# Kernel optimization log

Hardware: AMD Instinct MI355X
Metric: run time of the kernel (lower is better)

Reference implementation:

```python
import jax, jax.numpy as jnp
import numpy as np

B, C, H, W = 32, 3, 512, 512


def expm_affine(theta):
    # theta: [B, 2, 3] -> pad to 3x3 with a zero bottom row, matrix-exp, keep top 2 rows
    zero_row = jnp.zeros((theta.shape[0], 1, 3), theta.dtype)
    A = jnp.concatenate([theta, zero_row], axis=1)  # [B,3,3]
    E = jax.vmap(jax.scipy.linalg.expm)(A)
    return E[:, :2, :]


def affine_grid(theta23, h, w):
    # torch F.affine_grid with align_corners=False: pixel-center normalized coords
    xs = (2.0 * jnp.arange(w, dtype=theta23.dtype) + 1.0) / w - 1.0  # [W]
    ys = (2.0 * jnp.arange(h, dtype=theta23.dtype) + 1.0) / h - 1.0  # [H]
    gx, gy = jnp.meshgrid(xs, ys)  # [H,W] each
    base = jnp.stack([gx, gy, jnp.ones_like(gx)], axis=-1)  # [H,W,3]
    # grid[b,h,w,j] = sum_k theta[b,j,k] * base[h,w,k]; j=0 -> x, j=1 -> y
    return jnp.einsum('hwk,bjk->bhwj', base, theta23)  # [B,H,W,2]


def grid_sample(img, grid):
    # bilinear, zeros padding, align_corners=False (torch defaults)
    b, c, h, w = img.shape
    ix = (grid[..., 0] + 1.0) * (w * 0.5) - 0.5  # [B,Ho,Wo]
    iy = (grid[..., 1] + 1.0) * (h * 0.5) - 0.5
    x0 = jnp.floor(ix)
    y0 = jnp.floor(iy)
    x1, y1 = x0 + 1.0, y0 + 1.0
    wa = (x1 - ix) * (y1 - iy)
    wb = (x1 - ix) * (iy - y0)
    wc = (ix - x0) * (y1 - iy)
    wd = (ix - x0) * (iy - y0)

    def fetch(xf, yf):
        valid = (xf >= 0) & (xf <= w - 1) & (yf >= 0) & (yf <= h - 1)
        xc = jnp.clip(xf, 0, w - 1).astype(jnp.int32)
        yc = jnp.clip(yf, 0, h - 1).astype(jnp.int32)
        v = jax.vmap(lambda im, y, x: im[:, y, x])(img, yc, xc)  # [B,C,Ho,Wo]
        return v * valid[:, None].astype(img.dtype)

    out = (fetch(x0, y0) * wa[:, None]
           + fetch(x0, y1) * wb[:, None]
           + fetch(x1, y0) * wc[:, None]
           + fetch(x1, y1) * wd[:, None])
    return out


def setup_inputs() -> dict:
    key = jax.random.key(0)
    kx, kt = jax.random.split(key)
    x = jax.random.normal(kx, (B, C, H, W), dtype=jnp.float32)
    theta = jax.random.normal(kt, (B, 6), dtype=jnp.float32)
    return {"x": x, "theta": theta}


def reference(x, theta):
    th = theta.reshape(-1, 2, 3)
    A = expm_affine(th)            # [B,2,3]
    grid = affine_grid(A, H, W)    # [B,H,W,2]
    return grid_sample(x, grid)    # [B,C,H,W]
```

## Files before the change

kernel.cpp:

```cpp
#include <hip/hip_runtime.h>
#include <math.h>

#define BB 32
#define CC 3
#define HH 512
#define WW 512

typedef float vfloat4 __attribute__((ext_vector_type(4)));

__global__ void expm_kernel(const float* __restrict__ theta, float* __restrict__ E) {
    int b = threadIdx.x;
    if (b >= BB) return;

    double A[3][3];
#pragma unroll
    for (int j = 0; j < 2; ++j)
#pragma unroll
        for (int k = 0; k < 3; ++k)
            A[j][k] = (double)theta[b * 6 + j * 3 + k];
    A[2][0] = A[2][1] = A[2][2] = 0.0;

    double nrm = 0.0;
#pragma unroll
    for (int i = 0; i < 3; ++i) {
        double r = fabs(A[i][0]) + fabs(A[i][1]) + fabs(A[i][2]);
        nrm = fmax(nrm, r);
    }
    int s = 0;
    while (nrm > 0.5) { nrm *= 0.5; ++s; }
    double sc = ldexp(1.0, -s);
#pragma unroll
    for (int i = 0; i < 3; ++i)
#pragma unroll
        for (int k = 0; k < 3; ++k) A[i][k] *= sc;

    double R[3][3] = {{1, 0, 0}, {0, 1, 0}, {0, 0, 1}};
    double T[3][3] = {{1, 0, 0}, {0, 1, 0}, {0, 0, 1}};
    for (int k = 1; k <= 20; ++k) {
        double N[3][3];
        double inv = 1.0 / (double)k;
#pragma unroll
        for (int i = 0; i < 3; ++i)
#pragma unroll
            for (int j = 0; j < 3; ++j)
                N[i][j] = (T[i][0] * A[0][j] + T[i][1] * A[1][j] + T[i][2] * A[2][j]) * inv;
#pragma unroll
        for (int i = 0; i < 3; ++i)
#pragma unroll
            for (int j = 0; j < 3; ++j) {
                T[i][j] = N[i][j];
                R[i][j] += N[i][j];
            }
    }
    for (int q = 0; q < s; ++q) {
        double N[3][3];
#pragma unroll
        for (int i = 0; i < 3; ++i)
#pragma unroll
            for (int j = 0; j < 3; ++j)
                N[i][j] = R[i][0] * R[0][j] + R[i][1] * R[1][j] + R[i][2] * R[2][j];
#pragma unroll
        for (int i = 0; i < 3; ++i)
#pragma unroll
            for (int j = 0; j < 3; ++j) R[i][j] = N[i][j];
    }

#pragma unroll
    for (int j = 0; j < 2; ++j)
#pragma unroll
        for (int k = 0; k < 3; ++k)
            E[b * 6 + j * 3 + k] = (float)R[j][k];
}

__global__ __launch_bounds__(256) void st_sample_kernel(const float* __restrict__ x,
                                                        const float* __restrict__ E,
                                                        float* __restrict__ out) {
    const int b = blockIdx.x >> 8;
    const int tid_in_b = (blockIdx.x & 255) * 256 + threadIdx.x;
    const int wq = tid_in_b & (WW / 4 - 1);
    const int h = tid_in_b >> 7;

    const float t00 = E[b * 6 + 0], t01 = E[b * 6 + 1], t02 = E[b * 6 + 2];
    const float t10 = E[b * 6 + 3], t11 = E[b * 6 + 4], t12 = E[b * 6 + 5];

    const float gy = (2.0f * (float)h + 1.0f) * (1.0f / (float)HH) - 1.0f;
    const float* __restrict__ xb = x + (size_t)b * CC * HH * WW;

    float acc[CC][4];

#pragma unroll
    for (int j = 0; j < 4; ++j) {
        int w = wq * 4 + j;
        float gx = (2.0f * (float)w + 1.0f) * (1.0f / (float)WW) - 1.0f;
        float grid_x = t00 * gx + t01 * gy + t02;
        float grid_y = t10 * gx + t11 * gy + t12;
        float ix = (grid_x + 1.0f) * ((float)WW * 0.5f) - 0.5f;
        float iy = (grid_y + 1.0f) * ((float)HH * 0.5f) - 0.5f;

        bool any = (ix > -1.0f) & (ix < (float)WW) & (iy > -1.0f) & (iy < (float)HH);
        if (any) {
            float x0f = floorf(ix), y0f = floorf(iy);
            float x1f = x0f + 1.0f, y1f = y0f + 1.0f;
            float wa = (x1f - ix) * (y1f - iy);
            float wb = (x1f - ix) * (iy - y0f);
            float wc = (ix - x0f) * (y1f - iy);
            float wd = (ix - x0f) * (iy - y0f);

            float mx0 = (x0f >= 0.0f) ? 1.0f : 0.0f;
            float mx1 = (x1f <= (float)(WW - 1)) ? 1.0f : 0.0f;
            float my0 = (y0f >= 0.0f) ? 1.0f : 0.0f;
            float my1 = (y1f <= (float)(HH - 1)) ? 1.0f : 0.0f;

            int xi0 = (int)fminf(fmaxf(x0f, 0.0f), (float)(WW - 1));
            int xi1 = (int)fminf(fmaxf(x1f, 0.0f), (float)(WW - 1));
            int yi0 = (int)fminf(fmaxf(y0f, 0.0f), (float)(HH - 1));
            int yi1 = (int)fminf(fmaxf(y1f, 0.0f), (float)(HH - 1));

            float wA = wa * mx0 * my0;
            float wB = wb * mx0 * my1;
            float wC = wc * mx1 * my0;
            float wD = wd * mx1 * my1;

            int o00 = yi0 * WW + xi0;
            int o01 = yi1 * WW + xi0;
            int o10 = yi0 * WW + xi1;
            int o11 = yi1 * WW + xi1;

#pragma unroll
            for (int c = 0; c < CC; ++c) {
                const float* __restrict__ xc = xb + c * (HH * WW);
                acc[c][j] = wA * xc[o00] + wB * xc[o01] + wC * xc[o10] + wD * xc[o11];
            }
        } else {
#pragma unroll
            for (int c = 0; c < CC; ++c) acc[c][j] = 0.0f;
        }
    }

    size_t obase = ((size_t)b * CC) * (HH * WW) + (size_t)h * WW + (size_t)wq * 4;
#pragma unroll
    for (int c = 0; c < CC; ++c) {
        vfloat4 v = {acc[c][0], acc[c][1], acc[c][2], acc[c][3]};
        __builtin_nontemporal_store(v, reinterpret_cast<vfloat4*>(out + obase + (size_t)c * (HH * WW)));
    }
}

extern "C" void kernel_launch(void* const* d_in, const int* in_sizes, int n_in,
                              void* d_out, int out_size, void* d_ws, size_t ws_size,
                              hipStream_t stream) {
    const float* x = (const float*)d_in[0];
    const float* theta = (const float*)d_in[1];
    float* out = (float*)d_out;
    float* E = (float*)d_ws;

    expm_kernel<<<1, 64, 0, stream>>>(theta, E);

    const int total = BB * HH * (WW / 4);
    st_sample_kernel<<<total / 256, 256, 0, stream>>>(x, E, out);
}
```

Before: 247.0 us.

## Fetch bilinear neighbours as paired 8-byte loads and batch gathers per channel

The sampler now precomputes weights and base offsets for all four pixels, then reads each row's two horizontal neighbours with one 8-byte load instead of two scalar loads, selecting values by offset. When every lane in a wave has all samples in range, all gathers for a channel are issued together to raise memory-level parallelism. Otherwise a per-pixel fallback runs. The Taylor series in the expm kernel is also shortened to 14 terms and fully unrolled, which slightly changes the numerics of the affine matrix. The 8-byte loads may be misaligned, which can cost extra on some accesses.

```diff
diff --git a/kernel.cpp b/kernel.cpp
--- a/kernel.cpp
+++ b/kernel.cpp
@@ -8,6 +8,13 @@
 
 typedef float vfloat4 __attribute__((ext_vector_type(4)));
 
+struct f2 { float a, b; };
+__device__ __forceinline__ f2 load_f2(const float* __restrict__ p) {
+    f2 r;
+    __builtin_memcpy(&r, p, sizeof(f2));
+    return r;
+}
+
 __global__ void expm_kernel(const float* __restrict__ theta, float* __restrict__ E) {
     int b = threadIdx.x;
     if (b >= BB) return;
@@ -36,9 +43,10 @@
 
     double R[3][3] = {{1, 0, 0}, {0, 1, 0}, {0, 0, 1}};
     double T[3][3] = {{1, 0, 0}, {0, 1, 0}, {0, 0, 1}};
-    for (int k = 1; k <= 20; ++k) {
+#pragma unroll
+    for (int k = 1; k <= 14; ++k) {
         double N[3][3];
-        double inv = 1.0 / (double)k;
+        const double inv = 1.0 / (double)k;
 #pragma unroll
         for (int i = 0; i < 3; ++i)
 #pragma unroll
@@ -86,7 +94,9 @@
     const float gy = (2.0f * (float)h + 1.0f) * (1.0f / (float)HH) - 1.0f;
     const float* __restrict__ xb = x + (size_t)b * CC * HH * WW;
 
-    float acc[CC][4];
+    float wAa[4], wBa[4], wCa[4], wDa[4];
+    int ib0[4], ib1[4], d0a[4], d1a[4];
+    int anya[4];
 
 #pragma unroll
     for (int j = 0; j < 4; ++j) {
@@ -98,6 +108,7 @@
         float iy = (grid_y + 1.0f) * ((float)HH * 0.5f) - 0.5f;
 
         bool any = (ix > -1.0f) & (ix < (float)WW) & (iy > -1.0f) & (iy < (float)HH);
+        anya[j] = (int)any;
         if (any) {
             float x0f = floorf(ix), y0f = floorf(iy);
             float x1f = x0f + 1.0f, y1f = y0f + 1.0f;
@@ -116,24 +127,63 @@
             int yi0 = (int)fminf(fmaxf(y0f, 0.0f), (float)(HH - 1));
             int yi1 = (int)fminf(fmaxf(y1f, 0.0f), (float)(HH - 1));
 
-            float wA = wa * mx0 * my0;
-            float wB = wb * mx0 * my1;
-            float wC = wc * mx1 * my0;
-            float wD = wd * mx1 * my1;
-
-            int o00 = yi0 * WW + xi0;
-            int o01 = yi1 * WW + xi0;
-            int o10 = yi0 * WW + xi1;
-            int o11 = yi1 * WW + xi1;
-
-#pragma unroll
-            for (int c = 0; c < CC; ++c) {
-                const float* __restrict__ xc = xb + c * (HH * WW);
-                acc[c][j] = wA * xc[o00] + wB * xc[o01] + wC * xc[o10] + wD * xc[o11];
-            }
+            int bx = min(xi0, WW - 2);
+            d0a[j] = xi0 - bx;
+            d1a[j] = xi1 - bx;
+            ib0[j] = yi0 * WW + bx;
+            ib1[j] = yi1 * WW + bx;
+            wAa[j] = wa * mx0 * my0;
+            wBa[j] = wb * mx0 * my1;
+            wCa[j] = wc * mx1 * my0;
+            wDa[j] = wd * mx1 * my1;
         } else {
-#pragma unroll
-            for (int c = 0; c < CC; ++c) acc[c][j] = 0.0f;
+            wAa[j] = wBa[j] = wCa[j] = wDa[j] = 0.0f;
+            ib0[j] = ib1[j] = 0;
+            d0a[j] = d1a[j] = 0;
+        }
+    }
+
+    float acc[CC][4];
+
+    const bool all4 = anya[0] & anya[1] & anya[2] & anya[3];
+    if (__all((int)all4)) {
+#pragma unroll
+        for (int c = 0; c < CC; ++c) {
+            const float* __restrict__ xc = xb + c * (HH * WW);
+            f2 r0[4], r1[4];
+#pragma unroll
+            for (int j = 0; j < 4; ++j) {
+                r0[j] = load_f2(xc + ib0[j]);
+                r1[j] = load_f2(xc + ib1[j]);
+            }
+#pragma unroll
+            for (int j = 0; j < 4; ++j) {
+                float v00 = d0a[j] ? r0[j].b : r0[j].a;
+                float v10 = d1a[j] ? r0[j].b : r0[j].a;
+                float v01 = d0a[j] ? r1[j].b : r1[j].a;
+                float v11 = d1a[j] ? r1[j].b : r1[j].a;
+                acc[c][j] = wAa[j] * v00 + wBa[j] * v01 + wCa[j] * v10 + wDa[j] * v11;
+            }
+        }
+    } else {
+#pragma unroll
+        for (int j = 0; j < 4; ++j) {
+            if (anya[j]) {
+#pragma unroll
+                for (int c = 0; c < CC; ++c) {
+                    const float* __restrict__ xc = xb + c * (HH * WW);
+                    f2 r0 = load_f2(xc + ib0[j]);
+                    f2 r1 = load_f2(xc + ib1[j]);
+                    float v00 = d0a[j] ? r0.b : r0.a;
+                    float v10 = d1a[j] ? r0.b : r0.a;
+                    float v01 = d0a[j] ? r1.b : r1.a;
+                    float v11 = d1a[j] ? r1.b : r1.a;
+                    acc[c][j] = wAa[j] * v00 + wBa[j] * v01 + wCa[j] * v10 + wDa[j] * v11;
+                }
+            } else {
+#pragma unroll
+                for (int c = 0; c < CC; ++c) acc[c][j] = 0.0f;
+            }
         }
     }
 
```

Measured after the change: 217.9 us. -11.8%, faster.

## Tile output into 2D 8x8 wave patches and fetch bilinear pairs as float2

Applied to the files above, without the earlier changes.

Remaps each wave to an 8x8 output patch (16x16 per block), one pixel per thread, so the gathered source pixels of a wave are spatially compact under arbitrary affine warps and cache locality improves. The two horizontal neighbours are fetched with a single 8-byte load per row and channel, selecting between them by offset. It also shortens the Taylor series to 14 terms and unrolls it. In exchange, output stores become scalar, non-vectorized and no longer nontemporal, and the unaligned float2 loads may split.

```diff
diff --git a/kernel.cpp b/kernel.cpp
--- a/kernel.cpp
+++ b/kernel.cpp
@@ -6,7 +6,12 @@
 #define HH 512
 #define WW 512
 
-typedef float vfloat4 __attribute__((ext_vector_type(4)));
+struct f2 { float a, b; };
+__device__ __forceinline__ f2 load_f2(const float* __restrict__ p) {
+    f2 r;
+    __builtin_memcpy(&r, p, sizeof(f2));
+    return r;
+}
 
 __global__ void expm_kernel(const float* __restrict__ theta, float* __restrict__ E) {
     int b = threadIdx.x;
@@ -36,9 +41,10 @@
 
     double R[3][3] = {{1, 0, 0}, {0, 1, 0}, {0, 0, 1}};
     double T[3][3] = {{1, 0, 0}, {0, 1, 0}, {0, 0, 1}};
-    for (int k = 1; k <= 20; ++k) {
+#pragma unroll
+    for (int k = 1; k <= 14; ++k) {
         double N[3][3];
-        double inv = 1.0 / (double)k;
+        const double inv = 1.0 / (double)k;
 #pragma unroll
         for (int i = 0; i < 3; ++i)
 #pragma unroll
@@ -75,74 +81,81 @@
 __global__ __launch_bounds__(256) void st_sample_kernel(const float* __restrict__ x,
                                                         const float* __restrict__ E,
                                                         float* __restrict__ out) {
-    const int b = blockIdx.x >> 8;
-    const int tid_in_b = (blockIdx.x & 255) * 256 + threadIdx.x;
-    const int wq = tid_in_b & (WW / 4 - 1);
-    const int h = tid_in_b >> 7;
+    const int bid = blockIdx.x;
+    const int b = bid >> 10;
+    const int t = bid & 1023;
+    const int tileY = t >> 5, tileX = t & 31;
+
+    const int tid = threadIdx.x;
+    const int wv = tid >> 6, lane = tid & 63;
+    const int px = (tileX << 4) + ((wv & 1) << 3) + (lane & 7);
+    const int py = (tileY << 4) + ((wv >> 1) << 3) + (lane >> 3);
 
     const float t00 = E[b * 6 + 0], t01 = E[b * 6 + 1], t02 = E[b * 6 + 2];
     const float t10 = E[b * 6 + 3], t11 = E[b * 6 + 4], t12 = E[b * 6 + 5];
 
-    const float gy = (2.0f * (float)h + 1.0f) * (1.0f / (float)HH) - 1.0f;
     const float* __restrict__ xb = x + (size_t)b * CC * HH * WW;
 
-    float acc[CC][4];
+    const float gx = (2.0f * (float)px + 1.0f) * (1.0f / (float)WW) - 1.0f;
+    const float gy = (2.0f * (float)py + 1.0f) * (1.0f / (float)HH) - 1.0f;
+    const float grid_x = t00 * gx + t01 * gy + t02;
+    const float grid_y = t10 * gx + t11 * gy + t12;
+    const float ix = (grid_x + 1.0f) * ((float)WW * 0.5f) - 0.5f;
+    const float iy = (grid_y + 1.0f) * ((float)HH * 0.5f) - 0.5f;
 
+    float acc[CC] = {0.0f, 0.0f, 0.0f};
+
+    const bool any = (ix > -1.0f) & (ix < (float)WW) & (iy > -1.0f) & (iy < (float)HH);
+    if (any) {
+        float x0f = floorf(ix), y0f = floorf(iy);
+        float x1f = x0f + 1.0f, y1f = y0f + 1.0f;
+        float wa = (x1f - ix) * (y1f - iy);
+        float wb = (x1f - ix) * (iy - y0f);
+        float wc = (ix - x0f) * (y1f - iy);
+        float wd = (ix - x0f) * (iy - y0f);
+
+        float mx0 = (x0f >= 0.0f) ? 1.0f : 0.0f;
+        float mx1 = (x1f <= (float)(WW - 1)) ? 1.0f : 0.0f;
+        float my0 = (y0f >= 0.0f) ? 1.0f : 0.0f;
+        float my1 = (y1f <= (float)(HH - 1)) ? 1.0f : 0.0f;
+
+        int xi0 = (int)fminf(fmaxf(x0f, 0.0f), (float)(WW - 1));
+        int xi1 = (int)fminf(fmaxf(x1f, 0.0f), (float)(WW - 1));
+        int yi0 = (int)fminf(fmaxf(y0f, 0.0f), (float)(HH - 1));
+        int yi1 = (int)fminf(fmaxf(y1f, 0.0f), (float)(HH - 1));
+
+        int bx = min(xi0, WW - 2);
+        int d0 = xi0 - bx;
+        int d1 = xi1 - bx;
+        int ib0 = yi0 * WW + bx;
+        int ib1 = yi1 * WW + bx;
+
+        float wA = wa * mx0 * my0;
+        float wB = wb * mx0 * my1;
+        float wC = wc * mx1 * my0;
+        float wD = wd * mx1 * my1;
+
+        f2 r0[CC], r1[CC];
 #pragma unroll
-    for (int j = 0; j < 4; ++j) {
-        int w = wq * 4 + j;
-        float gx = (2.0f * (float)w + 1.0f) * (1.0f / (float)WW) - 1.0f;
-        float grid_x = t00 * gx + t01 * gy + t02;
-        float grid_y = t10 * gx + t11 * gy + t12;
-        float ix = (grid_x + 1.0f) * ((float)WW * 0.5f) - 0.5f;
-        float iy = (grid_y + 1.0f) * ((float)HH * 0.5f) - 0.5f;
-
-        bool any = (ix > -1.0f) & (ix < (float)WW) & (iy > -1.0f) & (iy < (float)HH);
-        if (any) {
-            float x0f = floorf(ix), y0f = floorf(iy);
-            float x1f = x0f + 1.0f, y1f = y0f + 1.0f;
-            float wa = (x1f - ix) * (y1f - iy);
-            float wb = (x1f - ix) * (iy - y0f);
-            float wc = (ix - x0f) * (y1f - iy);
-            float wd = (ix - x0f) * (iy - y0f);
-
-            float mx0 = (x0f >= 0.0f) ? 1.0f : 0.0f;
-            float mx1 = (x1f <= (float)(WW - 1)) ? 1.0f : 0.0f;
-            float my0 = (y0f >= 0.0f) ? 1.0f : 0.0f;
-            float my1 = (y1f <= (float)(HH - 1)) ? 1.0f : 0.0f;
-
-            int xi0 = (int)fminf(fmaxf(x0f, 0.0f), (float)(WW - 1));
-            int xi1 = (int)fminf(fmaxf(x1f, 0.0f), (float)(WW - 1));
-            int yi0 = (int)fminf(fmaxf(y0f, 0.0f), (float)(HH - 1));
-            int yi1 = (int)fminf(fmaxf(y1f, 0.0f), (float)(HH - 1));
-
-            float wA = wa * mx0 * my0;
-            float wB = wb * mx0 * my1;
-            float wC = wc * mx1 * my0;
-            float wD = wd * mx1 * my1;
-
-            int o00 = yi0 * WW + xi0;
-            int o01 = yi1 * WW + xi0;
-            int o10 = yi0 * WW + xi1;
-            int o11 = yi1 * WW + xi1;
-
+        for (int c = 0; c < CC; ++c) {
+            const float* __restrict__ xc = xb + c * (HH * WW);
+            r0[c] = load_f2(xc + ib0);
+            r1[c] = load_f2(xc + ib1);
+        }
 #pragma unroll
-            for (int c = 0; c < CC; ++c) {
-                const float* __restrict__ xc = xb + c * (HH * WW);
-                acc[c][j] = wA * xc[o00] + wB * xc[o01] + wC * xc[o10] + wD * xc[o11];
-            }
-        } else {
-#pragma unroll
-            for (int c = 0; c < CC; ++c) acc[c][j] = 0.0f;
+        for (int c = 0; c < CC; ++c) {
+            float v00 = d0 ? r0[c].b : r0[c].a;
+            float v10 = d1 ? r0[c].b : r0[c].a;
+            float v01 = d0 ? r1[c].b : r1[c].a;
+            float v11 = d1 ? r1[c].b : r1[c].a;
+            acc[c] = wA * v00 + wB * v01 + wC * v10 + wD * v11;
         }
     }
 
-    size_t obase = ((size_t)b * CC) * (HH * WW) + (size_t)h * WW + (size_t)wq * 4;
+    const size_t obase = ((size_t)b * CC) * (HH * WW) + (size_t)py * WW + px;
 #pragma unroll
-    for (int c = 0; c < CC; ++c) {
-        vfloat4 v = {acc[c][0], acc[c][1], acc[c][2], acc[c][3]};
-        __builtin_nontemporal_store(v, reinterpret_cast<vfloat4*>(out + obase + (size_t)c * (HH * WW)));
-    }
+    for (int c = 0; c < CC; ++c)
+        out[obase + (size_t)c * (HH * WW)] = acc[c];
 }
 
 extern "C" void kernel_launch(void* const* d_in, const int* in_sizes, int n_in,
@@ -155,6 +168,6 @@
 
     expm_kernel<<<1, 64, 0, stream>>>(theta, E);
 
-    const int total = BB * HH * (WW / 4);
-    st_sample_kernel<<<total / 256, 256, 0, stream>>>(x, E, out);
+    const int nblocks = BB * 32 * 32;
+    st_sample_kernel<<<nblocks, 256, 0, stream>>>(x, E, out);
 }
```

New measurement: 209.8 us. 1.18x faster.
